# Optimization experiments

Measured on AMD Instinct MI355X. Metric: run time of the kernel, lower is better.

The kernel has to match this reference:

```python
import jax, jax.numpy as jnp
import numpy as np
from jax import lax

NPOINTS = [1024, 256, 64, 16]
RADII = [0.02, 0.04, 0.06, 0.08]
NSAMPLE = [32, 32, 16, 16]
# per-level MLP widths; first entry already includes the +3 for use_xyz concat
MLPS = [[6, 32, 32, 64], [67, 64, 64, 128], [131, 128, 128, 256], [259, 256, 256, 512]]
EPS = 1e-5


def setup_inputs() -> dict:
    key = jax.random.key(0)
    B, N = 8, 16384
    pc = jax.random.uniform(jax.random.fold_in(key, 0), (B, N, 6), jnp.float32)
    # xyz into a 0.2-cube so the hard-coded radii (0.02..0.08) find real neighborhoods
    pc = pc.at[..., :3].multiply(0.2)
    inp = {"pointcloud": pc}
    ki = 1
    for l, m in enumerate(MLPS):
        for j in range(len(m) - 1):
            cin, cout = m[j], m[j + 1]
            inp[f"w{l}{j}"] = jax.random.normal(jax.random.fold_in(key, ki), (cin, cout), jnp.float32) * (1.0 / float(np.sqrt(cin)))
            inp[f"g{l}{j}"] = jnp.ones((cout,), jnp.float32)
            inp[f"b{l}{j}"] = jnp.zeros((cout,), jnp.float32)
            ki += 1
    return inp


def _fps(xyz, npoint):
    # iterative farthest point sampling, start at index 0 (matches CUDA kernel)
    B, N, _ = xyz.shape

    def step(carry, _):
        mind, last = carry
        lastp = jnp.take_along_axis(xyz, last[:, None, None], axis=1)  # [B,1,3]
        d = jnp.sum((xyz - lastp) ** 2, axis=-1)                       # [B,N]
        mind = jnp.minimum(mind, d)
        nxt = jnp.argmax(mind, axis=1).astype(jnp.int32)
        return (mind, nxt), last

    init = (jnp.full((B, N), 1e10, xyz.dtype), jnp.zeros((B,), jnp.int32))
    _, idx = lax.scan(step, init, None, length=npoint)
    return jnp.transpose(idx)  # [B,npoint]


def _gather(pts, idx):
    # pts [B,N,C], idx [B,...] -> [B,...,C]
    return jax.vmap(lambda p, i: p[i])(pts, idx)


def _ball_query(xyz, centers, radius, nsample):
    # first nsample points (in index order) within radius; pad with first hit (0 if none)
    N = xyz.shape[1]
    d2 = jnp.sum((centers[:, :, None, :] - xyz[:, None, :, :]) ** 2, axis=-1)  # [B,S,N]
    key = jnp.where(d2 < radius * radius, jnp.arange(N, dtype=jnp.int32), N)
    negtop, _ = lax.top_k(-key, nsample)
    sel = -negtop                      # ascending candidate indices
    valid = sel < N
    first = jnp.where(valid[..., :1], sel[..., :1], 0)
    return jnp.where(valid, sel, first)  # [B,S,nsample] int32


def _sa(xyz, feats, npoint, radius, nsample, layers):
    fps_idx = lax.stop_gradient(_fps(xyz, npoint))
    new_xyz = _gather(xyz, fps_idx)                    # [B,S,3]
    idx = _ball_query(xyz, new_xyz, radius, nsample)   # [B,S,K]
    g = _gather(xyz, idx) - new_xyz[:, :, None, :]     # centered grouped xyz [B,S,K,3]
    g = jnp.concatenate([g, _gather(feats, idx)], axis=-1)  # use_xyz concat -> [B,S,K,3+C]
    x = g
    for W, gamma, beta in layers:
        x = jnp.einsum('bski,io->bsko', x, W)          # 1x1 conv, bias=False (bn on)
        mu = jnp.mean(x, axis=(0, 1, 2))               # BN training-mode batch stats
        var = jnp.var(x, axis=(0, 1, 2))
        x = jax.nn.relu(gamma * (x - mu) * lax.rsqrt(var + EPS) + beta)
    return new_xyz, jnp.max(x, axis=2)                 # max-pool over neighbors -> [B,S,Cout]


def reference(pointcloud, w00, g00, b00, w01, g01, b01, w02, g02, b02,
              w10, g10, b10, w11, g11, b11, w12, g12, b12,
              w20, g20, b20, w21, g21, b21, w22, g22, b22,
              w30, g30, b30, w31, g31, b31, w32, g32, b32):
    params = [
        [(w00, g00, b00), (w01, g01, b01), (w02, g02, b02)],
        [(w10, g10, b10), (w11, g11, b11), (w12, g12, b12)],
        [(w20, g20, b20), (w21, g21, b21), (w22, g22, b22)],
        [(w30, g30, b30), (w31, g31, b31), (w32, g32, b32)],
    ]
    xyz = pointcloud[..., :3]
    feats = pointcloud[..., 3:]   # channels-last (torch keeps [B,C,N]; pure layout diff)
    l_xyz, l_feats = [xyz], [feats]
    for k in range(4):
        nx, nf = _sa(l_xyz[k], l_feats[k], NPOINTS[k], RADII[k], NSAMPLE[k], params[k])
        l_xyz.append(nx)
        l_feats.append(nf)
    return tuple(l_xyz) + tuple(l_feats)
```

## Files before the change

### kernel.cpp

```cpp
#include <hip/hip_runtime.h>

#define WAVE 64

__global__ __launch_bounds__(256) void split_zero_kernel(const float* __restrict__ pc,
    float* __restrict__ xyz, float* __restrict__ feats, int total,
    float* __restrict__ stats, int n_stats) {
  int t = blockIdx.x * blockDim.x + threadIdx.x;
  if (t < n_stats) stats[t] = 0.f;
  if (t >= total) return;
  const float* p = pc + (size_t)t * 6;
  xyz[t * 3 + 0] = p[0]; xyz[t * 3 + 1] = p[1]; xyz[t * 3 + 2] = p[2];
  feats[t * 3 + 0] = p[3]; feats[t * 3 + 1] = p[4]; feats[t * 3 + 2] = p[5];
}

__device__ __forceinline__ float dpp_max_f32(float v) {
#define DPP_STEP_F(ctrl) { int t_ = __builtin_amdgcn_update_dpp( \
      __float_as_int(v), __float_as_int(v), ctrl, 0xf, 0xf, false); \
    v = fmaxf(v, __int_as_float(t_)); }
  DPP_STEP_F(0x111) DPP_STEP_F(0x112) DPP_STEP_F(0x114)
  DPP_STEP_F(0x118) DPP_STEP_F(0x142) DPP_STEP_F(0x143)
#undef DPP_STEP_F
  return v;
}
__device__ __forceinline__ unsigned dpp_max_u32(unsigned v) {
#define DPP_STEP_U(ctrl) { unsigned t_ = (unsigned)__builtin_amdgcn_update_dpp( \
      (int)v, (int)v, ctrl, 0xf, 0xf, false); \
    v = (t_ > v) ? t_ : v; }
  DPP_STEP_U(0x111) DPP_STEP_U(0x112) DPP_STEP_U(0x114)
  DPP_STEP_U(0x118) DPP_STEP_U(0x142) DPP_STEP_U(0x143)
#undef DPP_STEP_U
  return v;
}
__device__ __forceinline__ unsigned bcast63(unsigned v) {
  return (unsigned)__builtin_amdgcn_readlane((int)v, 63);
}

__global__ __launch_bounds__(1024, 4) void fps_big_kernel(const float* __restrict__ xyz,
    float* __restrict__ new_xyz, int N, int S) {
  const int b = blockIdx.x;
  const int tid = threadIdx.x;
  const int lane = tid & 63;
  const float* px = xyz + (size_t)b * N * 3;
  __shared__ unsigned long long s_key[3];
  float rx[16], ry[16], rz[16], mind[16];
#pragma unroll
  for (int p = 0; p < 16; ++p) {
    int i = tid + p * 1024;
    rx[p] = px[i * 3 + 0]; ry[p] = px[i * 3 + 1]; rz[p] = px[i * 3 + 2];
    asm volatile("" : "+v"(rx[p]), "+v"(ry[p]), "+v"(rz[p]));
    mind[p] = 1e10f;
  }
  if (tid < 3) s_key[tid] = 0ull;
  float qx = px[0], qy = px[1], qz = px[2];
  if (tid == 0) {
    float* o = new_xyz + (size_t)b * S * 3;
    o[0] = qx; o[1] = qy; o[2] = qz;
  }
  __syncthreads();
  for (unsigned it = 1; it < (unsigned)S; ++it) {
    float bestv = -1.f; unsigned besti = 0;
#pragma unroll
    for (int p = 0; p < 16; ++p) {
      float dx = __fsub_rn(rx[p], qx);
      float dy = __fsub_rn(ry[p], qy);
      float dz = __fsub_rn(rz[p], qz);
      float d = __fadd_rn(__fadd_rn(__fmul_rn(dx, dx), __fmul_rn(dy, dy)), __fmul_rn(dz, dz));
      float mo = fminf(mind[p], d);
      mind[p] = mo;
      if (mo > bestv) { bestv = mo; besti = (unsigned)(tid + p * 1024); }
    }
    float wm = dpp_max_f32(bestv);
    unsigned wmb = bcast63(__float_as_uint(wm));
    unsigned cand = (__float_as_uint(bestv) == wmb) ? (0xFFFFFFFFu - besti) : 0u;
    unsigned winv = bcast63(dpp_max_u32(cand));
    if (lane == 0) atomicMax(&s_key[it % 3u], ((unsigned long long)wmb << 32) | winv);
    if (tid == 0) s_key[(it + 1) % 3u] = 0ull;
    __syncthreads();
    unsigned long long k = s_key[it % 3u];
    int last = (int)(0xFFFFFFFFu - (unsigned)k);
    const float* q = px + (size_t)last * 3;
    qx = q[0]; qy = q[1]; qz = q[2];
    if (tid == 0) {
      float* o = new_xyz + ((size_t)b * S + it) * 3;
      o[0] = qx; o[1] = qy; o[2] = qz;
    }
  }
}

__global__ void fps_small_kernel(const float* __restrict__ xyz,
    float* __restrict__ new_xyz, int N, int S) {
  const int b = blockIdx.x;
  const int tid = threadIdx.x;
  const int lane = tid & 63;
  const float* px = xyz + (size_t)b * N * 3;
  __shared__ float sx[1024], sy[1024], sz[1024];
  __shared__ unsigned long long s_key[3];
  float x = px[tid * 3 + 0], y = px[tid * 3 + 1], z = px[tid * 3 + 2];
  sx[tid] = x; sy[tid] = y; sz[tid] = z;
  if (tid < 3) s_key[tid] = 0ull;
  float mind = 1e10f;
  float qx = px[0], qy = px[1], qz = px[2];
  if (tid == 0) {
    float* o = new_xyz + (size_t)b * S * 3;
    o[0] = qx; o[1] = qy; o[2] = qz;
  }
  __syncthreads();
  for (unsigned it = 1; it < (unsigned)S; ++it) {
    float dx = __fsub_rn(x, qx);
    float dy = __fsub_rn(y, qy);
    float dz = __fsub_rn(z, qz);
    float d = __fadd_rn(__fadd_rn(__fmul_rn(dx, dx), __fmul_rn(dy, dy)), __fmul_rn(dz, dz));
    mind = fminf(mind, d);
    float wm = dpp_max_f32(mind);
    unsigned wmb = bcast63(__float_as_uint(wm));
    unsigned cand = (__float_as_uint(mind) == wmb) ? (0xFFFFFFFFu - (unsigned)tid) : 0u;
    unsigned winv = bcast63(dpp_max_u32(cand));
    if (lane == 0) atomicMax(&s_key[it % 3u], ((unsigned long long)wmb << 32) | winv);
    if (tid == 0) s_key[(it + 1) % 3u] = 0ull;
    __syncthreads();
    unsigned long long k = s_key[it % 3u];
    int last = (int)(0xFFFFFFFFu - (unsigned)k);
    qx = sx[last]; qy = sy[last]; qz = sz[last];
    if (tid == 0) {
      float* o = new_xyz + ((size_t)b * S + it) * 3;
      o[0] = qx; o[1] = qy; o[2] = qz;
    }
  }
}

__global__ __launch_bounds__(256) void ballgroup_kernel(const float* __restrict__ xyz,
    const float* __restrict__ feats, const float* __restrict__ centers,
    float* __restrict__ X, int N, int S, int K, int ci, float r2) {
  __shared__ int s_sel[4][32];
  const int wid = threadIdx.x >> 6;
  const int lane = threadIdx.x & 63;
  const int gw = blockIdx.x * 4 + wid;
  const int b = gw / S;
  const float* px = xyz + (size_t)b * N * 3;
  const float* cp = centers + (size_t)gw * 3;
  float cx = cp[0], cy = cp[1], cz = cp[2];
  int cnt = 0;
  int firsti = 0;
  for (int base = 0; base < N; base += WAVE) {
    int i = base + lane;
    float dx = __fsub_rn(cx, px[i * 3 + 0]);
    float dy = __fsub_rn(cy, px[i * 3 + 1]);
    float dz = __fsub_rn(cz, px[i * 3 + 2]);
    float d = __fadd_rn(__fadd_rn(__fmul_rn(dx, dx), __fmul_rn(dy, dy)), __fmul_rn(dz, dz));
    bool hit = d < r2;
    unsigned long long m = __ballot(hit);
    if (hit) {
      int slot = cnt + __popcll(m & ((1ull << lane) - 1ull));
      if (slot < K) s_sel[wid][slot] = i;
    }
    if (cnt == 0 && m) firsti = base + __ffsll((unsigned long long)m) - 1;
    cnt += __popcll(m);
    if (cnt >= K) break;
  }
  for (int q = cnt + lane; q < K; q += WAVE) s_sel[wid][q] = firsti;
  __syncthreads();
  const int C0 = ci + 3;
  const float* pf = feats + (size_t)b * N * ci;
  float* Xg = X + (size_t)gw * K * C0;
  for (int k = 0; k < K; ++k) {
    int j = s_sel[wid][k];
    const float* fj = pf + (size_t)j * ci;
    float* xr = Xg + (size_t)k * C0;
    float jx = px[j * 3 + 0], jy = px[j * 3 + 1], jz = px[j * 3 + 2];
    for (int c = lane; c < C0; c += WAVE) {
      float v;
      if (c == 0)      v = __fsub_rn(jx, cx);
      else if (c == 1) v = __fsub_rn(jy, cy);
      else if (c == 2) v = __fsub_rn(jz, cz);
      else             v = fj[c - 3];
      xr[c] = v;
    }
  }
}

#define BM 64
#define BN 64
#define BK 16
__global__ __launch_bounds__(256) void mm_fused_kernel(const float* __restrict__ A,
    const float* __restrict__ W, float* __restrict__ Y,
    float* __restrict__ st_out, const float* __restrict__ st_in,
    const float* __restrict__ g_in, const float* __restrict__ b_in,
    int R, int C, int Co, float inv_n) {
  __shared__ float As[BK][BM + 4];
  __shared__ float Bs[BK][BN + 4];
  __shared__ float s_mu[260], s_rs[260], s_g[260], s_b[260];
  __shared__ float s_sum[BN], s_sq[BN];
  int r0 = blockIdx.x * BM;
  int n0 = blockIdx.y * BN;
  int tid = threadIdx.x;
  int tx = tid & 15, ty = tid >> 4;
  if (st_in) {
    for (int c = tid; c < C; c += 256) {
      float mu = st_in[c] * inv_n;
      float var = st_in[512 + c] * inv_n - mu * mu;
      s_mu[c] = mu; s_rs[c] = rsqrtf(var + 1e-5f);
      s_g[c] = g_in[c]; s_b[c] = b_in[c];
    }
  }
  if (tid < BN) { s_sum[tid] = 0.f; s_sq[tid] = 0.f; }
  __syncthreads();
  float acc[4][4] = {};
  for (int k0 = 0; k0 < C; k0 += BK) {
#pragma unroll
    for (int u = 0; u < 4; ++u) {
      int lin = tid + u * 256;
      int row = lin >> 4;
      int cc = lin & 15;
      int c = k0 + cc;
      float v = 0.f;
      if (c < C) {
        v = A[(size_t)(r0 + row) * C + c];
        if (st_in) {
          v = s_g[c] * ((v - s_mu[c]) * s_rs[c]) + s_b[c];
          v = v > 0.f ? v : 0.f;
        }
      }
      As[cc][row] = v;
    }
#pragma unroll
    for (int u = 0; u < 4; ++u) {
      int lin = tid + u * 256;
      int kk = lin >> 6;
      int n = lin & 63;
      int c = k0 + kk;
      Bs[kk][n] = (c < C && (n0 + n) < Co) ? W[(size_t)c * Co + n0 + n] : 0.f;
    }
    __syncthreads();
#pragma unroll
    for (int kk = 0; kk < BK; ++kk) {
      float a0[4], b0[4];
#pragma unroll
      for (int i = 0; i < 4; ++i) a0[i] = As[kk][ty * 4 + i];
#pragma unroll
      for (int jj = 0; jj < 4; ++jj) b0[jj] = Bs[kk][tx * 4 + jj];
#pragma unroll
      for (int i = 0; i < 4; ++i)
#pragma unroll
        for (int jj = 0; jj < 4; ++jj)
          acc[i][jj] = fmaf(a0[i], b0[jj], acc[i][jj]);
    }
    __syncthreads();
  }
#pragma unroll
  for (int i = 0; i < 4; ++i) {
    int r = r0 + ty * 4 + i;
#pragma unroll
    for (int jj = 0; jj < 4; ++jj) {
      int n = n0 + tx * 4 + jj;
      if (n < Co) Y[(size_t)r * Co + n] = acc[i][jj];
    }
  }
#pragma unroll
  for (int jj = 0; jj < 4; ++jj) {
    float cs = 0.f, cq = 0.f;
#pragma unroll
    for (int i = 0; i < 4; ++i) { float v = acc[i][jj]; cs += v; cq += v * v; }
    atomicAdd(&s_sum[tx * 4 + jj], cs);
    atomicAdd(&s_sq[tx * 4 + jj], cq);
  }
  __syncthreads();
  if (tid < BN) {
    int n = n0 + tid;
    if (n < Co) {
      atomicAdd(&st_out[n], s_sum[tid]);
      atomicAdd(&st_out[512 + n], s_sq[tid]);
    }
  }
}

__global__ __launch_bounds__(256) void norm_relu_max_kernel(const float* __restrict__ Y,
    float* __restrict__ O, const float* __restrict__ st,
    const float* __restrict__ gamma, const float* __restrict__ beta,
    int G, int K, int Co, float inv_n) {
  int t = blockIdx.x * blockDim.x + threadIdx.x;
  if (t >= G * Co) return;
  int c = t & (Co - 1);
  int g = t / Co;
  float mu = st[c] * inv_n;
  float var = st[512 + c] * inv_n - mu * mu;
  float rs = rsqrtf(var + 1e-5f);
  float ga = gamma[c], be = beta[c];
  const float* yp = Y + (size_t)g * K * Co + c;
  float m = -1e30f;
  for (int k = 0; k < K; ++k) {
    float v = ga * ((yp[(size_t)k * Co] - mu) * rs) + be;
    m = fmaxf(m, v);
  }
  O[t] = m > 0.f ? m : 0.f;
}

extern "C" void kernel_launch(void* const* d_in, const int* in_sizes, int n_in,
                              void* d_out, int out_size, void* d_ws, size_t ws_size,
                              hipStream_t stream) {
  const float* pc = (const float*)d_in[0];
  float* out = (float*)d_out;
  char* wsb = (char*)d_ws;

  float* stats = (float*)(wsb + ((size_t)1 << 20));
  float* bufA = (float*)(wsb + ((size_t)3 << 20));
  float* bufB = (float*)(wsb + ((size_t)37 << 20));

  const int B = 8;
  static const int Ns[4] = {16384, 1024, 256, 64};
  static const int Ss[4] = {1024, 256, 64, 16};
  static const int Ks[4] = {32, 32, 16, 16};
  static const double Rr[4] = {0.02, 0.04, 0.06, 0.08};
  static const int Ci[4] = {3, 64, 128, 256};
  static const int mlp[4][4] = {{6,32,32,64},{67,64,64,128},{131,128,128,256},{259,256,256,512}};
  static const size_t ox[5] = {0, 393216, 417792, 423936, 425472};
  static const size_t of[5] = {425856, 819072, 1343360, 1605504, 1736576};

  split_zero_kernel<<<(B * 16384 + 255) / 256, 256, 0, stream>>>(
      pc, out + ox[0], out + of[0], B * 16384, stats, 12 * 1024);

  for (int l = 0; l < 4; ++l) {
    const float* xyz = out + ox[l];
    const float* fts = out + of[l];
    float* nxyz = out + ox[l + 1];
    const int N = Ns[l], S = Ss[l], K = Ks[l], ci = Ci[l], C0 = ci + 3;
    const float r2 = (float)(Rr[l] * Rr[l]);

    if (l == 0) fps_big_kernel<<<B, 1024, 0, stream>>>(xyz, nxyz, N, S);
    else        fps_small_kernel<<<B, N, 0, stream>>>(xyz, nxyz, N, S);

    ballgroup_kernel<<<(B * S) / 4, 256, 0, stream>>>(xyz, fts, nxyz, bufA,
                                                      N, S, K, ci, r2);

    const int R = B * S * K;
    const float inv_n = 1.0f / (float)R;
    float* X = bufA; float* Y = bufB;
    const float* prev_st = nullptr;
    const float* prev_g = nullptr;
    const float* prev_b = nullptr;
    for (int j = 0; j < 3; ++j) {
      const int cin = mlp[l][j], cout = mlp[l][j + 1];
      const float* Wt = (const float*)d_in[1 + (l * 3 + j) * 3 + 0];
      const float* Ga = (const float*)d_in[1 + (l * 3 + j) * 3 + 1];
      const float* Be = (const float*)d_in[1 + (l * 3 + j) * 3 + 2];
      float* st = stats + (size_t)(l * 3 + j) * 1024;
      dim3 grid(R / 64, (cout + 63) / 64);
      mm_fused_kernel<<<grid, 256, 0, stream>>>(X, Wt, Y, st, prev_st, prev_g, prev_b,
                                                R, cin, cout, inv_n);
      if (j < 2) {
        prev_st = st; prev_g = Ga; prev_b = Be;
        float* tswap = X; X = Y; Y = tswap;
      } else {
        int G = B * S;
        int tot = G * cout;
        norm_relu_max_kernel<<<(tot + 255) / 256, 256, 0, stream>>>(Y, out + of[l + 1], st, Ga, Be,
                                                                    G, K, cout, inv_n);
      }
    }
  }
}
```

Measured before the change: 2.858 ms.

## Fuse all FPS levels into one kernel and each SA level into a persistent grid-barrier kernel

All four farthest-point-sampling levels now run inside one kernel per batch. Levels two to four read the previous level's centers from shared memory instead of reloading them from global memory. Each set-abstraction level (ball query, grouping, three GEMMs with fused BN stats, normalize-relu-max) becomes one persistent kernel with 256 blocks separated by software grid barriers. This cuts kernel launches and lets later FPS levels avoid extra launches. In exchange, each stage is capped at 256 blocks, barriers spin on global atomics, and correctness depends on all blocks being co-resident.

```diff
diff --git a/kernel.cpp b/kernel.cpp
--- a/kernel.cpp
+++ b/kernel.cpp
@@ -1,6 +1,10 @@
 #include <hip/hip_runtime.h>
 
 #define WAVE 64
+#define BM 64
+#define BN 64
+#define BK 16
+#define NBLK 256
 
 __global__ __launch_bounds__(256) void split_zero_kernel(const float* __restrict__ pc,
     float* __restrict__ xyz, float* __restrict__ feats, int total,
@@ -35,74 +39,19 @@
   return (unsigned)__builtin_amdgcn_readlane((int)v, 63);
 }
 
-__global__ __launch_bounds__(1024, 4) void fps_big_kernel(const float* __restrict__ xyz,
-    float* __restrict__ new_xyz, int N, int S) {
-  const int b = blockIdx.x;
+template<int NPTS>
+__device__ void fps_level(const float* sx, const float* sy, const float* sz,
+    int S, float* outp, float* mx, float* my, float* mz,
+    unsigned long long* s_key) {
   const int tid = threadIdx.x;
   const int lane = tid & 63;
-  const float* px = xyz + (size_t)b * N * 3;
-  __shared__ unsigned long long s_key[3];
-  float rx[16], ry[16], rz[16], mind[16];
-#pragma unroll
-  for (int p = 0; p < 16; ++p) {
-    int i = tid + p * 1024;
-    rx[p] = px[i * 3 + 0]; ry[p] = px[i * 3 + 1]; rz[p] = px[i * 3 + 2];
-    asm volatile("" : "+v"(rx[p]), "+v"(ry[p]), "+v"(rz[p]));
-    mind[p] = 1e10f;
-  }
+  float x = sx[tid & (NPTS - 1)], y = sy[tid & (NPTS - 1)], z = sz[tid & (NPTS - 1)];
+  float mind = (tid < NPTS) ? 1e10f : 0.0f;
   if (tid < 3) s_key[tid] = 0ull;
-  float qx = px[0], qy = px[1], qz = px[2];
+  float qx = sx[0], qy = sy[0], qz = sz[0];
   if (tid == 0) {
-    float* o = new_xyz + (size_t)b * S * 3;
-    o[0] = qx; o[1] = qy; o[2] = qz;
-  }
-  __syncthreads();
-  for (unsigned it = 1; it < (unsigned)S; ++it) {
-    float bestv = -1.f; unsigned besti = 0;
-#pragma unroll
-    for (int p = 0; p < 16; ++p) {
-      float dx = __fsub_rn(rx[p], qx);
-      float dy = __fsub_rn(ry[p], qy);
-      float dz = __fsub_rn(rz[p], qz);
-      float d = __fadd_rn(__fadd_rn(__fmul_rn(dx, dx), __fmul_rn(dy, dy)), __fmul_rn(dz, dz));
-      float mo = fminf(mind[p], d);
-      mind[p] = mo;
-      if (mo > bestv) { bestv = mo; besti = (unsigned)(tid + p * 1024); }
-    }
-    float wm = dpp_max_f32(bestv);
-    unsigned wmb = bcast63(__float_as_uint(wm));
-    unsigned cand = (__float_as_uint(bestv) == wmb) ? (0xFFFFFFFFu - besti) : 0u;
-    unsigned winv = bcast63(dpp_max_u32(cand));
-    if (lane == 0) atomicMax(&s_key[it % 3u], ((unsigned long long)wmb << 32) | winv);
-    if (tid == 0) s_key[(it + 1) % 3u] = 0ull;
-    __syncthreads();
-    unsigned long long k = s_key[it % 3u];
-    int last = (int)(0xFFFFFFFFu - (unsigned)k);
-    const float* q = px + (size_t)last * 3;
-    qx = q[0]; qy = q[1]; qz = q[2];
-    if (tid == 0) {
-      float* o = new_xyz + ((size_t)b * S + it) * 3;
-      o[0] = qx; o[1] = qy; o[2] = qz;
-    }
-  }
-}
-
-__global__ void fps_small_kernel(const float* __restrict__ xyz,
-    float* __restrict__ new_xyz, int N, int S) {
-  const int b = blockIdx.x;
-  const int tid = threadIdx.x;
-  const int lane = tid & 63;
-  const float* px = xyz + (size_t)b * N * 3;
-  __shared__ float sx[1024], sy[1024], sz[1024];
-  __shared__ unsigned long long s_key[3];
-  float x = px[tid * 3 + 0], y = px[tid * 3 + 1], z = px[tid * 3 + 2];
-  sx[tid] = x; sy[tid] = y; sz[tid] = z;
-  if (tid < 3) s_key[tid] = 0ull;
-  float mind = 1e10f;
-  float qx = px[0], qy = px[1], qz = px[2];
-  if (tid == 0) {
-    float* o = new_xyz + (size_t)b * S * 3;
-    o[0] = qx; o[1] = qy; o[2] = qz;
+    outp[0] = qx; outp[1] = qy; outp[2] = qz;
+    if (mx) { mx[0] = qx; my[0] = qy; mz[0] = qz; }
   }
   __syncthreads();
   for (unsigned it = 1; it < (unsigned)S; ++it) {
@@ -122,78 +71,100 @@
     int last = (int)(0xFFFFFFFFu - (unsigned)k);
     qx = sx[last]; qy = sy[last]; qz = sz[last];
     if (tid == 0) {
-      float* o = new_xyz + ((size_t)b * S + it) * 3;
+      float* o = outp + (size_t)it * 3;
       o[0] = qx; o[1] = qy; o[2] = qz;
-    }
-  }
-}
-
-__global__ __launch_bounds__(256) void ballgroup_kernel(const float* __restrict__ xyz,
-    const float* __restrict__ feats, const float* __restrict__ centers,
-    float* __restrict__ X, int N, int S, int K, int ci, float r2) {
-  __shared__ int s_sel[4][32];
-  const int wid = threadIdx.x >> 6;
-  const int lane = threadIdx.x & 63;
-  const int gw = blockIdx.x * 4 + wid;
-  const int b = gw / S;
-  const float* px = xyz + (size_t)b * N * 3;
-  const float* cp = centers + (size_t)gw * 3;
-  float cx = cp[0], cy = cp[1], cz = cp[2];
-  int cnt = 0;
-  int firsti = 0;
-  for (int base = 0; base < N; base += WAVE) {
-    int i = base + lane;
-    float dx = __fsub_rn(cx, px[i * 3 + 0]);
-    float dy = __fsub_rn(cy, px[i * 3 + 1]);
-    float dz = __fsub_rn(cz, px[i * 3 + 2]);
-    float d = __fadd_rn(__fadd_rn(__fmul_rn(dx, dx), __fmul_rn(dy, dy)), __fmul_rn(dz, dz));
-    bool hit = d < r2;
-    unsigned long long m = __ballot(hit);
-    if (hit) {
-      int slot = cnt + __popcll(m & ((1ull << lane) - 1ull));
-      if (slot < K) s_sel[wid][slot] = i;
-    }
-    if (cnt == 0 && m) firsti = base + __ffsll((unsigned long long)m) - 1;
-    cnt += __popcll(m);
-    if (cnt >= K) break;
-  }
-  for (int q = cnt + lane; q < K; q += WAVE) s_sel[wid][q] = firsti;
+      if (mx) { mx[it] = qx; my[it] = qy; mz[it] = qz; }
+    }
+  }
   __syncthreads();
-  const int C0 = ci + 3;
-  const float* pf = feats + (size_t)b * N * ci;
-  float* Xg = X + (size_t)gw * K * C0;
-  for (int k = 0; k < K; ++k) {
-    int j = s_sel[wid][k];
-    const float* fj = pf + (size_t)j * ci;
-    float* xr = Xg + (size_t)k * C0;
-    float jx = px[j * 3 + 0], jy = px[j * 3 + 1], jz = px[j * 3 + 2];
-    for (int c = lane; c < C0; c += WAVE) {
-      float v;
-      if (c == 0)      v = __fsub_rn(jx, cx);
-      else if (c == 1) v = __fsub_rn(jy, cy);
-      else if (c == 2) v = __fsub_rn(jz, cz);
-      else             v = fj[c - 3];
-      xr[c] = v;
-    }
-  }
-}
-
-#define BM 64
-#define BN 64
-#define BK 16
-__global__ __launch_bounds__(256) void mm_fused_kernel(const float* __restrict__ A,
-    const float* __restrict__ W, float* __restrict__ Y,
-    float* __restrict__ st_out, const float* __restrict__ st_in,
-    const float* __restrict__ g_in, const float* __restrict__ b_in,
-    int R, int C, int Co, float inv_n) {
-  __shared__ float As[BK][BM + 4];
-  __shared__ float Bs[BK][BN + 4];
-  __shared__ float s_mu[260], s_rs[260], s_g[260], s_b[260];
-  __shared__ float s_sum[BN], s_sq[BN];
-  int r0 = blockIdx.x * BM;
-  int n0 = blockIdx.y * BN;
-  int tid = threadIdx.x;
-  int tx = tid & 15, ty = tid >> 4;
+}
+
+__global__ __launch_bounds__(1024, 4) void fps_mega_kernel(const float* __restrict__ xyz,
+    float* __restrict__ nx1, float* __restrict__ nx2, float* __restrict__ nx3,
+    float* __restrict__ nx4) {
+  const int b = blockIdx.x;
+  const int tid = threadIdx.x;
+  const int lane = tid & 63;
+  __shared__ float s_ax[1024], s_ay[1024], s_az[1024];
+  __shared__ float s_bx[256], s_by[256], s_bz[256];
+  __shared__ unsigned long long s_key[3];
+  const float* px = xyz + (size_t)b * 16384 * 3;
+  {
+    float rx[16], ry[16], rz[16], mind[16];
+#pragma unroll
+    for (int p = 0; p < 16; ++p) {
+      int i = tid + p * 1024;
+      rx[p] = px[i * 3 + 0]; ry[p] = px[i * 3 + 1]; rz[p] = px[i * 3 + 2];
+      asm volatile("" : "+v"(rx[p]), "+v"(ry[p]), "+v"(rz[p]));
+      mind[p] = 1e10f;
+    }
+    if (tid < 3) s_key[tid] = 0ull;
+    float qx = px[0], qy = px[1], qz = px[2];
+    if (tid == 0) {
+      float* o = nx1 + (size_t)b * 1024 * 3;
+      o[0] = qx; o[1] = qy; o[2] = qz;
+      s_ax[0] = qx; s_ay[0] = qy; s_az[0] = qz;
+    }
+    __syncthreads();
+    for (unsigned it = 1; it < 1024u; ++it) {
+      float bestv = -1.f; unsigned besti = 0;
+#pragma unroll
+      for (int p = 0; p < 16; ++p) {
+        float dx = __fsub_rn(rx[p], qx);
+        float dy = __fsub_rn(ry[p], qy);
+        float dz = __fsub_rn(rz[p], qz);
+        float d = __fadd_rn(__fadd_rn(__fmul_rn(dx, dx), __fmul_rn(dy, dy)), __fmul_rn(dz, dz));
+        float mo = fminf(mind[p], d);
+        mind[p] = mo;
+        if (mo > bestv) { bestv = mo; besti = (unsigned)(tid + p * 1024); }
+      }
+      float wm = dpp_max_f32(bestv);
+      unsigned wmb = bcast63(__float_as_uint(wm));
+      unsigned cand = (__float_as_uint(bestv) == wmb) ? (0xFFFFFFFFu - besti) : 0u;
+      unsigned winv = bcast63(dpp_max_u32(cand));
+      if (lane == 0) atomicMax(&s_key[it % 3u], ((unsigned long long)wmb << 32) | winv);
+      if (tid == 0) s_key[(it + 1) % 3u] = 0ull;
+      __syncthreads();
+      unsigned long long k = s_key[it % 3u];
+      int last = (int)(0xFFFFFFFFu - (unsigned)k);
+      const float* q = px + (size_t)last * 3;
+      qx = q[0]; qy = q[1]; qz = q[2];
+      if (tid == 0) {
+        float* o = nx1 + ((size_t)b * 1024 + it) * 3;
+        o[0] = qx; o[1] = qy; o[2] = qz;
+        s_ax[it] = qx; s_ay[it] = qy; s_az[it] = qz;
+      }
+    }
+    __syncthreads();
+  }
+  fps_level<1024>(s_ax, s_ay, s_az, 256, nx2 + (size_t)b * 256 * 3,
+                  s_bx, s_by, s_bz, s_key);
+  fps_level<256>(s_bx, s_by, s_bz, 64, nx3 + (size_t)b * 64 * 3,
+                 s_ax, s_ay, s_az, s_key);
+  fps_level<64>(s_ax, s_ay, s_az, 16, nx4 + (size_t)b * 16 * 3,
+                nullptr, nullptr, nullptr, s_key);
+}
+
+__device__ __forceinline__ void grid_barrier(unsigned long long* cnt, unsigned stage) {
+  __syncthreads();
+  if (threadIdx.x == 0) {
+    __threadfence();
+    __hip_atomic_fetch_add(cnt, 1ull, __ATOMIC_RELEASE, __HIP_MEMORY_SCOPE_AGENT);
+    unsigned long long tgt = (unsigned long long)gridDim.x * stage;
+    while (__hip_atomic_load(cnt, __ATOMIC_ACQUIRE, __HIP_MEMORY_SCOPE_AGENT) < tgt)
+      __builtin_amdgcn_s_sleep(2);
+    __threadfence();
+  }
+  __syncthreads();
+}
+
+__device__ void gemm_stage(const float* A, const float* W, float* Y,
+    float* st_out, const float* st_in, const float* g_in, const float* b_in,
+    int R, int C, int Co, float inv_n,
+    float (*As)[BM + 4], float (*Bs)[BN + 4],
+    float* s_mu, float* s_rs, float* s_g, float* s_b,
+    float* s_sum, float* s_sq) {
+  const int tid = threadIdx.x;
   if (st_in) {
     for (int c = tid; c < C; c += 256) {
       float mu = st_in[c] * inv_n;
@@ -202,96 +173,187 @@
       s_g[c] = g_in[c]; s_b[c] = b_in[c];
     }
   }
-  if (tid < BN) { s_sum[tid] = 0.f; s_sq[tid] = 0.f; }
-  __syncthreads();
-  float acc[4][4] = {};
-  for (int k0 = 0; k0 < C; k0 += BK) {
-#pragma unroll
-    for (int u = 0; u < 4; ++u) {
-      int lin = tid + u * 256;
-      int row = lin >> 4;
-      int cc = lin & 15;
-      int c = k0 + cc;
-      float v = 0.f;
-      if (c < C) {
-        v = A[(size_t)(r0 + row) * C + c];
-        if (st_in) {
-          v = s_g[c] * ((v - s_mu[c]) * s_rs[c]) + s_b[c];
-          v = v > 0.f ? v : 0.f;
+  const int nrt = R >> 6;
+  const int nct = (Co + 63) >> 6;
+  const int ntiles = nrt * nct;
+  const int tx = tid & 15, ty = tid >> 4;
+  for (int tile = blockIdx.x; tile < ntiles; tile += gridDim.x) {
+    int r0 = (tile % nrt) * BM;
+    int n0 = (tile / nrt) * BN;
+    __syncthreads();
+    if (tid < BN) { s_sum[tid] = 0.f; s_sq[tid] = 0.f; }
+    __syncthreads();
+    float acc[4][4] = {};
+    for (int k0 = 0; k0 < C; k0 += BK) {
+#pragma unroll
+      for (int u = 0; u < 4; ++u) {
+        int lin = tid + u * 256;
+        int row = lin >> 4;
+        int cc = lin & 15;
+        int c = k0 + cc;
+        float v = 0.f;
+        if (c < C) {
+          v = A[(size_t)(r0 + row) * C + c];
+          if (st_in) {
+            v = s_g[c] * ((v - s_mu[c]) * s_rs[c]) + s_b[c];
+            v = v > 0.f ? v : 0.f;
+          }
         }
-      }
-      As[cc][row] = v;
-    }
-#pragma unroll
-    for (int u = 0; u < 4; ++u) {
-      int lin = tid + u * 256;
-      int kk = lin >> 6;
-      int n = lin & 63;
-      int c = k0 + kk;
-      Bs[kk][n] = (c < C && (n0 + n) < Co) ? W[(size_t)c * Co + n0 + n] : 0.f;
-    }
-    __syncthreads();
-#pragma unroll
-    for (int kk = 0; kk < BK; ++kk) {
-      float a0[4], b0[4];
-#pragma unroll
-      for (int i = 0; i < 4; ++i) a0[i] = As[kk][ty * 4 + i];
-#pragma unroll
-      for (int jj = 0; jj < 4; ++jj) b0[jj] = Bs[kk][tx * 4 + jj];
-#pragma unroll
-      for (int i = 0; i < 4; ++i)
-#pragma unroll
-        for (int jj = 0; jj < 4; ++jj)
-          acc[i][jj] = fmaf(a0[i], b0[jj], acc[i][jj]);
-    }
-    __syncthreads();
-  }
-#pragma unroll
-  for (int i = 0; i < 4; ++i) {
-    int r = r0 + ty * 4 + i;
+        As[cc][row] = v;
+      }
+#pragma unroll
+      for (int u = 0; u < 4; ++u) {
+        int lin = tid + u * 256;
+        int kk = lin >> 6;
+        int n = lin & 63;
+        int c = k0 + kk;
+        Bs[kk][n] = (c < C && (n0 + n) < Co) ? W[(size_t)c * Co + n0 + n] : 0.f;
+      }
+      __syncthreads();
+#pragma unroll
+      for (int kk = 0; kk < BK; ++kk) {
+        float a0[4], b0[4];
+#pragma unroll
+        for (int i = 0; i < 4; ++i) a0[i] = As[kk][ty * 4 + i];
+#pragma unroll
+        for (int jj = 0; jj < 4; ++jj) b0[jj] = Bs[kk][tx * 4 + jj];
+#pragma unroll
+        for (int i = 0; i < 4; ++i)
+#pragma unroll
+          for (int jj = 0; jj < 4; ++jj)
+            acc[i][jj] = fmaf(a0[i], b0[jj], acc[i][jj]);
+      }
+      __syncthreads();
+    }
+#pragma unroll
+    for (int i = 0; i < 4; ++i) {
+      int r = r0 + ty * 4 + i;
+#pragma unroll
+      for (int jj = 0; jj < 4; ++jj) {
+        int n = n0 + tx * 4 + jj;
+        if (n < Co) Y[(size_t)r * Co + n] = acc[i][jj];
+      }
+    }
 #pragma unroll
     for (int jj = 0; jj < 4; ++jj) {
-      int n = n0 + tx * 4 + jj;
-      if (n < Co) Y[(size_t)r * Co + n] = acc[i][jj];
-    }
-  }
-#pragma unroll
-  for (int jj = 0; jj < 4; ++jj) {
-    float cs = 0.f, cq = 0.f;
-#pragma unroll
-    for (int i = 0; i < 4; ++i) { float v = acc[i][jj]; cs += v; cq += v * v; }
-    atomicAdd(&s_sum[tx * 4 + jj], cs);
-    atomicAdd(&s_sq[tx * 4 + jj], cq);
-  }
-  __syncthreads();
-  if (tid < BN) {
-    int n = n0 + tid;
-    if (n < Co) {
-      atomicAdd(&st_out[n], s_sum[tid]);
-      atomicAdd(&st_out[512 + n], s_sq[tid]);
-    }
-  }
-}
-
-__global__ __launch_bounds__(256) void norm_relu_max_kernel(const float* __restrict__ Y,
-    float* __restrict__ O, const float* __restrict__ st,
-    const float* __restrict__ gamma, const float* __restrict__ beta,
-    int G, int K, int Co, float inv_n) {
-  int t = blockIdx.x * blockDim.x + threadIdx.x;
-  if (t >= G * Co) return;
-  int c = t & (Co - 1);
-  int g = t / Co;
-  float mu = st[c] * inv_n;
-  float var = st[512 + c] * inv_n - mu * mu;
-  float rs = rsqrtf(var + 1e-5f);
-  float ga = gamma[c], be = beta[c];
-  const float* yp = Y + (size_t)g * K * Co + c;
-  float m = -1e30f;
-  for (int k = 0; k < K; ++k) {
-    float v = ga * ((yp[(size_t)k * Co] - mu) * rs) + be;
-    m = fmaxf(m, v);
-  }
-  O[t] = m > 0.f ? m : 0.f;
+      float cs = 0.f, cq = 0.f;
+#pragma unroll
+      for (int i = 0; i < 4; ++i) { float v = acc[i][jj]; cs += v; cq += v * v; }
+      atomicAdd(&s_sum[tx * 4 + jj], cs);
+      atomicAdd(&s_sq[tx * 4 + jj], cq);
+    }
+    __syncthreads();
+    if (tid < BN) {
+      int n = n0 + tid;
+      if (n < Co) {
+        atomicAdd(&st_out[n], s_sum[tid]);
+        atomicAdd(&st_out[512 + n], s_sq[tid]);
+      }
+    }
+  }
+}
+
+__global__ __launch_bounds__(256, 4) void layer_chain_kernel(
+    const float* __restrict__ xyz, const float* __restrict__ feats,
+    const float* __restrict__ centers, int* __restrict__ ballidx,
+    float* __restrict__ bufA, float* __restrict__ bufB, float* __restrict__ outF,
+    const float* __restrict__ W0, const float* __restrict__ g0, const float* __restrict__ b0,
+    const float* __restrict__ W1, const float* __restrict__ g1, const float* __restrict__ b1,
+    const float* __restrict__ W2, const float* __restrict__ g2, const float* __restrict__ b2,
+    float* __restrict__ stats, unsigned long long* __restrict__ bar,
+    int N, int S, int K, int ci, int c1, int c2, int c3, float r2, float inv_n) {
+  __shared__ float As[BK][BM + 4];
+  __shared__ float Bs[BK][BN + 4];
+  __shared__ float s_mu[260], s_rs[260], s_g[260], s_b[260];
+  __shared__ float s_sum[BN], s_sq[BN];
+  const int tid = threadIdx.x;
+  const int C0 = ci + 3;
+  const int R = 8 * S * K;
+  float* st0 = stats;
+  float* st1 = stats + 1024;
+  float* st2 = stats + 2048;
+
+  {
+    const int gwave = (blockIdx.x * 256 + tid) >> 6;
+    const int lane = tid & 63;
+    const int nw = gridDim.x * 4;
+    const int SG = 8 * S;
+    for (int g = gwave; g < SG; g += nw) {
+      int b = g / S;
+      const float* px = xyz + (size_t)b * N * 3;
+      const float* cp = centers + (size_t)g * 3;
+      float cx = cp[0], cy = cp[1], cz = cp[2];
+      int* outi = ballidx + (size_t)g * K;
+      int cnt = 0, firsti = 0;
+      for (int base = 0; base < N; base += WAVE) {
+        int i = base + lane;
+        float dx = __fsub_rn(cx, px[i * 3 + 0]);
+        float dy = __fsub_rn(cy, px[i * 3 + 1]);
+        float dz = __fsub_rn(cz, px[i * 3 + 2]);
+        float d = __fadd_rn(__fadd_rn(__fmul_rn(dx, dx), __fmul_rn(dy, dy)), __fmul_rn(dz, dz));
+        bool hit = d < r2;
+        unsigned long long m = __ballot(hit);
+        if (hit) {
+          int slot = cnt + __popcll(m & ((1ull << lane) - 1ull));
+          if (slot < K) outi[slot] = i;
+        }
+        if (cnt == 0 && m) firsti = base + __ffsll((unsigned long long)m) - 1;
+        cnt += __popcll(m);
+        if (cnt >= K) break;
+      }
+      for (int q = cnt + lane; q < K; q += WAVE) outi[q] = firsti;
+    }
+  }
+  grid_barrier(bar, 1);
+
+  {
+    long long total = (long long)R * C0;
+    for (long long t = (long long)blockIdx.x * 256 + tid; t < total;
+         t += (long long)gridDim.x * 256) {
+      int r = (int)(t / C0);
+      int c = (int)(t - (long long)r * C0);
+      int g = r / K;
+      int b = g / S;
+      int j = ballidx[r];
+      float v;
+      if (c < 3) v = __fsub_rn(xyz[((size_t)b * N + j) * 3 + c], centers[(size_t)g * 3 + c]);
+      else       v = feats[((size_t)b * N + j) * ci + (c - 3)];
+      bufA[(size_t)r * C0 + c] = v;
+    }
+  }
+  grid_barrier(bar, 2);
+
+  gemm_stage(bufA, W0, bufB, st0, nullptr, nullptr, nullptr, R, C0, c1, inv_n,
+             As, Bs, s_mu, s_rs, s_g, s_b, s_sum, s_sq);
+  grid_barrier(bar, 3);
+  gemm_stage(bufB, W1, bufA, st1, st0, g0, b0, R, c1, c2, inv_n,
+             As, Bs, s_mu, s_rs, s_g, s_b, s_sum, s_sq);
+  grid_barrier(bar, 4);
+  gemm_stage(bufA, W2, bufB, st2, st1, g1, b1, R, c2, c3, inv_n,
+             As, Bs, s_mu, s_rs, s_g, s_b, s_sum, s_sq);
+  grid_barrier(bar, 5);
+
+  {
+    const int Gc = 8 * S;
+    const int lc3 = 31 - __clz(c3);
+    long long tot = (long long)Gc << lc3;
+    for (long long t = (long long)blockIdx.x * 256 + tid; t < tot;
+         t += (long long)gridDim.x * 256) {
+      int c = (int)(t & (c3 - 1));
+      int g = (int)(t >> lc3);
+      float mu = st2[c] * inv_n;
+      float var = st2[512 + c] * inv_n - mu * mu;
+      float rs = rsqrtf(var + 1e-5f);
+      float ga = g2[c], be = b2[c];
+      const float* yp = bufB + (size_t)g * K * c3 + c;
+      float m = -1e30f;
+      for (int k = 0; k < K; ++k) {
+        float v = ga * ((yp[(size_t)k * c3] - mu) * rs) + be;
+        m = fmaxf(m, v);
+      }
+      outF[t] = m > 0.f ? m : 0.f;
+    }
+  }
 }
 
 extern "C" void kernel_launch(void* const* d_in, const int* in_sizes, int n_in,
@@ -301,7 +363,9 @@
   float* out = (float*)d_out;
   char* wsb = (char*)d_ws;
 
+  int* ballidx = (int*)wsb;
   float* stats = (float*)(wsb + ((size_t)1 << 20));
+  unsigned long long* barcnt = (unsigned long long*)(stats + 12 * 1024);
   float* bufA = (float*)(wsb + ((size_t)3 << 20));
   float* bufB = (float*)(wsb + ((size_t)37 << 20));
 
@@ -316,45 +380,23 @@
   static const size_t of[5] = {425856, 819072, 1343360, 1605504, 1736576};
 
   split_zero_kernel<<<(B * 16384 + 255) / 256, 256, 0, stream>>>(
-      pc, out + ox[0], out + of[0], B * 16384, stats, 12 * 1024);
+      pc, out + ox[0], out + of[0], B * 16384, stats, 12 * 1024 + 8);
+
+  fps_mega_kernel<<<B, 1024, 0, stream>>>(out + ox[0], out + ox[1], out + ox[2],
+                                          out + ox[3], out + ox[4]);
 
   for (int l = 0; l < 4; ++l) {
-    const float* xyz = out + ox[l];
-    const float* fts = out + of[l];
-    float* nxyz = out + ox[l + 1];
-    const int N = Ns[l], S = Ss[l], K = Ks[l], ci = Ci[l], C0 = ci + 3;
+    const int N = Ns[l], S = Ss[l], K = Ks[l], ci = Ci[l];
     const float r2 = (float)(Rr[l] * Rr[l]);
-
-    if (l == 0) fps_big_kernel<<<B, 1024, 0, stream>>>(xyz, nxyz, N, S);
-    else        fps_small_kernel<<<B, N, 0, stream>>>(xyz, nxyz, N, S);
-
-    ballgroup_kernel<<<(B * S) / 4, 256, 0, stream>>>(xyz, fts, nxyz, bufA,
-                                                      N, S, K, ci, r2);
-
     const int R = B * S * K;
     const float inv_n = 1.0f / (float)R;
-    float* X = bufA; float* Y = bufB;
-    const float* prev_st = nullptr;
-    const float* prev_g = nullptr;
-    const float* prev_b = nullptr;
-    for (int j = 0; j < 3; ++j) {
-      const int cin = mlp[l][j], cout = mlp[l][j + 1];
-      const float* Wt = (const float*)d_in[1 + (l * 3 + j) * 3 + 0];
-      const float* Ga = (const float*)d_in[1 + (l * 3 + j) * 3 + 1];
-      const float* Be = (const float*)d_in[1 + (l * 3 + j) * 3 + 2];
-      float* st = stats + (size_t)(l * 3 + j) * 1024;
-      dim3 grid(R / 64, (cout + 63) / 64);
-      mm_fused_kernel<<<grid, 256, 0, stream>>>(X, Wt, Y, st, prev_st, prev_g, prev_b,
-                                                R, cin, cout, inv_n);
-      if (j < 2) {
-        prev_st = st; prev_g = Ga; prev_b = Be;
-        float* tswap = X; X = Y; Y = tswap;
-      } else {
-        int G = B * S;
-        int tot = G * cout;
-        norm_relu_max_kernel<<<(tot + 255) / 256, 256, 0, stream>>>(Y, out + of[l + 1], st, Ga, Be,
-                                                                    G, K, cout, inv_n);
-      }
-    }
-  }
-}
+    const float** wp = (const float**)alloca(9 * sizeof(float*));
+    for (int j = 0; j < 9; ++j) wp[j] = (const float*)d_in[1 + l * 9 + j];
+    layer_chain_kernel<<<NBLK, 256, 0, stream>>>(
+        out + ox[l], out + of[l], out + ox[l + 1], ballidx, bufA, bufB,
+        out + of[l + 1],
+        wp[0], wp[1], wp[2], wp[3], wp[4], wp[5], wp[6], wp[7], wp[8],
+        stats + (size_t)l * 3 * 1024, barcnt + l,
+        N, S, K, ci, mlp[l][1], mlp[l][2], mlp[l][3], r2, inv_n);
+  }
+}
```

Result: slower. 4.620 ms (+61.7%).
